# Kernel tuning notes

Measured on AMD Instinct MI355X. Metric: run time of the kernel, lower is better.

Reference implementation:

```python
import jax, jax.numpy as jnp
import numpy as np

NUM_GRAPHS = 1024


def setup_inputs() -> dict:
    key = jax.random.key(0)
    k1, k2, k3, k4 = jax.random.split(key, 4)
    N, D, H = 500000, 256, 128
    x = jax.random.normal(k1, (N, D), dtype=jnp.float32)
    # attention MLP params (Linear(D,H) -> ReLU -> Linear(H,1))
    W1 = jax.random.normal(k2, (D, H), dtype=jnp.float32) * (1.0 / np.sqrt(D))
    b1 = jnp.zeros((H,), dtype=jnp.float32)
    W2 = jax.random.normal(k3, (H, 1), dtype=jnp.float32) * (1.0 / np.sqrt(H))
    b2 = jnp.zeros((1,), dtype=jnp.float32)
    batch = jnp.sort(jax.random.randint(k4, (N,), 0, NUM_GRAPHS)).astype(jnp.int64)
    return {"x": x, "W1": W1, "b1": b1, "W2": W2, "b2": b2, "batch": batch}


def reference(x, W1, b1, W2, b2, batch):
    # attention MLP -> scalar score per node, softmax over ALL nodes (global, as in source)
    h = jax.nn.relu(x @ W1 + b1)            # [N, H]
    scores = h @ W2 + b2                    # [N, 1]
    attn = jax.nn.softmax(scores.ravel())[:, None]  # [N, 1], global softmax

    # attention-weighted sum per graph
    attn_pooled = jax.ops.segment_sum(x * attn, batch, num_segments=NUM_GRAPHS,
                                      indices_are_sorted=True)  # [G, D]
    # max pool per graph (all segments occupied given N >> G)
    max_pooled = jax.ops.segment_max(x, batch, num_segments=NUM_GRAPHS,
                                     indices_are_sorted=True)   # [G, D]
    # mean pool per graph: scatter-add + clamped counts
    sum_pooled = jax.ops.segment_sum(x, batch, num_segments=NUM_GRAPHS,
                                     indices_are_sorted=True)   # [G, D]
    counts = jnp.bincount(batch, length=NUM_GRAPHS).astype(x.dtype)
    counts = jnp.clip(counts, 1.0, None)[:, None]                # [G, 1]
    mean_pooled = sum_pooled / counts

    return jnp.concatenate([attn_pooled, max_pooled, mean_pooled], axis=-1)  # [G, 3D]
```

## Files before the change

kernel.cpp:

```cpp
#include <hip/hip_runtime.h>
#include <cmath>

#define D_IN 256
#define H_DIM 128
#define NUM_GRAPHS 1024
#define CHUNK 32
#define MAXSEG 2
#define REC_F 768

typedef __attribute__((ext_vector_type(8))) __bf16 bf16x8;
typedef __attribute__((ext_vector_type(4))) float f32x4;

__device__ inline void load_lds_16(const void* g, void* l) {
    __builtin_amdgcn_global_load_lds(
        (const __attribute__((address_space(1))) void*)g,
        (__attribute__((address_space(3))) void*)l, 16, 0, 0);
}

__device__ inline int lower_bound_i(const int* __restrict__ arr, int n, int val) {
    int lo = 0, hi = n;
    while (lo < hi) {
        int mid = (lo + hi) >> 1;
        if (arr[mid] < val) lo = mid + 1; else hi = mid;
    }
    return lo;
}

__global__ __launch_bounds__(256) void prep_kernel(
    const float* __restrict__ W1, const int* __restrict__ batch, int N,
    ushort* __restrict__ packed, int* __restrict__ bounds) {
    int b = blockIdx.x;
    if (b < 16) {
        int tid = b * 256 + threadIdx.x;
        int nt = tid >> 9;
        int ks = (tid >> 6) & 7;
        int l = tid & 63;
        int col = nt * 16 + (l & 15);
        int kbase = ks * 32 + ((l >> 4) & 3) * 8;
#pragma unroll
        for (int i = 0; i < 8; ++i) {
            float v = W1[(size_t)(kbase + i) * H_DIM + col];
            __bf16 h = (__bf16)v;
            packed[(size_t)tid * 8 + i] = __builtin_bit_cast(unsigned short, h);
        }
    } else {
        int i = (b - 16) * 256 + threadIdx.x;
        if (i <= NUM_GRAPHS) bounds[i] = lower_bound_i(batch, N, i);
    }
}

__global__ __launch_bounds__(256, 4) void fused_kernel(
    const float* __restrict__ x, const ushort* __restrict__ w1p,
    const float* __restrict__ b1, const float* __restrict__ W2,
    const float* __restrict__ b2, const int* __restrict__ batch,
    float* __restrict__ recs, float* __restrict__ zpart, int N) {
    int tid = threadIdx.x;
    int l = tid & 63;
    int w = tid >> 6;
    int r16 = l & 15;
    int kg = l >> 4;
    int blk = blockIdx.x;
    long long base = (long long)blk * CHUNK;
    int chunkN = (int)min((long long)CHUNK, (long long)N - base);

    __shared__ float sxf[CHUNK * D_IN];
    __shared__ float pscore[4][CHUNK];
    __shared__ int seglist[MAXSEG + 1];
    __shared__ int snseg;

#pragma unroll
    for (int k = 0; k < 8; ++k) {
        int row = k * 4 + w;
        long long grow = base + row;
        if (grow >= N) grow = N - 1;
        unsigned srcb = ((unsigned)(l * 16)) ^ ((unsigned)(row & 7) << 4);
        const float* src = x + grow * D_IN + (srcb >> 2);
        char* dst = (char*)sxf + (unsigned)(row * 1024 + l * 16);
        load_lds_16(src, dst);
    }

    bf16x8 breg0[8], breg1[8];
#pragma unroll
    for (int ks = 0; ks < 8; ++ks) {
        breg0[ks] = *(const bf16x8*)(w1p + ((size_t)((w * 2) * 8 + ks) * 64 + l) * 8);
        breg1[ks] = *(const bf16x8*)(w1p + ((size_t)((w * 2 + 1) * 8 + ks) * 64 + l) * 8);
    }

    if (w == 0) {
        int bval = -1;
        if (l < chunkN) bval = batch[base + l];
        int prev = __shfl_up(bval, 1, 64);
        bool flag = (l < chunkN) && (l == 0 || bval != prev);
        unsigned long long m = __ballot(flag);
        if (l == 0) {
            int ns = 0;
            while (m && ns < MAXSEG) {
                seglist[ns] = __ffsll(m) - 1;
                ns++;
                m &= m - 1;
            }
            snseg = ns;
            seglist[ns] = chunkN;
        }
    }

    float w2v[2], b1v[2];
#pragma unroll
    for (int q = 0; q < 2; ++q) {
        int c = (w * 2 + q) * 16 + r16;
        w2v[q] = W2[c];
        b1v[q] = b1[c];
    }
    float bb = b2[0];

    __syncthreads();

    f32x4 acc[2][2] = {};
#pragma unroll
    for (int ks = 0; ks < 8; ++ks) {
#pragma unroll
        for (int mt = 0; mt < 2; ++mt) {
            int row = mt * 16 + r16;
            unsigned swz = (unsigned)(row & 7) << 4;
            unsigned cb = (unsigned)(ks * 128 + kg * 32);
            f32x4 u0 = *(const f32x4*)((const char*)sxf + row * 1024 + (cb ^ swz));
            f32x4 u1 = *(const f32x4*)((const char*)sxf + row * 1024 + ((cb + 16) ^ swz));
            bf16x8 af;
#pragma unroll
            for (int i = 0; i < 4; ++i) {
                af[i] = (__bf16)u0[i];
                af[i + 4] = (__bf16)u1[i];
            }
            acc[mt][0] = __builtin_amdgcn_mfma_f32_16x16x32_bf16(af, breg0[ks], acc[mt][0], 0, 0, 0);
            acc[mt][1] = __builtin_amdgcn_mfma_f32_16x16x32_bf16(af, breg1[ks], acc[mt][1], 0, 0, 0);
        }
    }
#pragma unroll
    for (int mt = 0; mt < 2; ++mt) {
#pragma unroll
        for (int reg = 0; reg < 4; ++reg) {
            float p = fmaxf(acc[mt][0][reg] + b1v[0], 0.f) * w2v[0] +
                      fmaxf(acc[mt][1][reg] + b1v[1], 0.f) * w2v[1];
            p += __shfl_xor(p, 1, 64);
            p += __shfl_xor(p, 2, 64);
            p += __shfl_xor(p, 4, 64);
            p += __shfl_xor(p, 8, 64);
            if (r16 == 0) pscore[w][mt * 16 + kg * 4 + reg] = p;
        }
    }
    __syncthreads();

    float e_l = 0.f;
    if (l < CHUNK) {
        float s = pscore[0][l] + pscore[1][l] + pscore[2][l] + pscore[3][l] + bb;
        e_l = (l < chunkN) ? __expf(s) : 0.f;
    }
    if (w == 0) {
        float z = e_l;
        z += __shfl_xor(z, 1, 64);
        z += __shfl_xor(z, 2, 64);
        z += __shfl_xor(z, 4, 64);
        z += __shfl_xor(z, 8, 64);
        z += __shfl_xor(z, 16, 64);
        z += __shfl_xor(z, 32, 64);
        if (l == 0) zpart[blk] = z;
    }

    int nseg = snseg;

    int cg = l & 15;
    int rg = l >> 4;
    unsigned cbyte = (unsigned)(w * 256 + cg * 16);

    for (int sg = 0; sg < nseg; ++sg) {
        int sStart = seglist[sg];
        int sEnd = seglist[sg + 1];
        f32x4 asum = {0.f, 0.f, 0.f, 0.f};
        f32x4 ssum = {0.f, 0.f, 0.f, 0.f};
        f32x4 mx = {-INFINITY, -INFINITY, -INFINITY, -INFINITY};
#pragma unroll
        for (int j = 0; j < 8; ++j) {
            int row = rg + 4 * j;
            float wj = __shfl(e_l, row, 64);
            bool in = (row >= sStart) && (row < sEnd);
            unsigned addr = (unsigned)(row * 1024) +
                            (cbyte ^ ((unsigned)(row & 7) << 4));
            f32x4 v = *(const f32x4*)((const char*)sxf + addr);
            float wje = in ? wj : 0.f;
#pragma unroll
            for (int c = 0; c < 4; ++c) {
                asum[c] += v[c] * wje;
                ssum[c] += in ? v[c] : 0.f;
                mx[c] = fmaxf(mx[c], in ? v[c] : -INFINITY);
            }
        }
#pragma unroll
        for (int c = 0; c < 4; ++c) {
            asum[c] += __shfl_xor(asum[c], 16, 64);
            asum[c] += __shfl_xor(asum[c], 32, 64);
            ssum[c] += __shfl_xor(ssum[c], 16, 64);
            ssum[c] += __shfl_xor(ssum[c], 32, 64);
            mx[c] = fmaxf(mx[c], __shfl_xor(mx[c], 16, 64));
            mx[c] = fmaxf(mx[c], __shfl_xor(mx[c], 32, 64));
        }
        if (rg == 0) {
            float* rb = recs + (size_t)(blk * MAXSEG + sg) * REC_F;
            int co = w * 64 + cg * 4;
            *(f32x4*)(rb + co) = asum;
            *(f32x4*)(rb + 256 + co) = ssum;
            *(f32x4*)(rb + 512 + co) = mx;
        }
    }
}

__global__ __launch_bounds__(256) void combine_kernel(
    const float* __restrict__ recs, const int* __restrict__ bounds,
    const int* __restrict__ batch, const float* __restrict__ zpart, int nzp,
    float* __restrict__ out) {
    int g = blockIdx.x;
    int tid = threadIdx.x;

    __shared__ float szr[256];
    float z = 0.f;
    for (int i = tid; i < nzp; i += 256) z += zpart[i];
    szr[tid] = z;
    __syncthreads();
    for (int off = 128; off > 0; off >>= 1) {
        if (tid < off) szr[tid] += szr[tid + off];
        __syncthreads();
    }
    float invZ = 1.f / szr[0];

    int start = bounds[g];
    int end = bounds[g + 1];
    int cnt = end - start;

    float ew = 0.f, ss = 0.f, mxv = -INFINITY;
    if (cnt > 0) {
        int b0 = start / CHUNK, b1 = (end - 1) / CHUNK;
        int sg0 = (batch[(long long)b0 * CHUNK] == g) ? 0 : 1;
        for (int b = b0; b <= b1; ++b) {
            int sg = (b == b0) ? sg0 : 0;
            const float* rb = recs + (size_t)(b * MAXSEG + sg) * REC_F;
            ew += rb[tid];
            ss += rb[256 + tid];
            mxv = fmaxf(mxv, rb[512 + tid]);
        }
    }
    size_t ob = (size_t)g * (3 * D_IN);
    out[ob + tid] = ew * invZ;
    out[ob + D_IN + tid] = (cnt > 0) ? mxv : 0.f;
    out[ob + 2 * D_IN + tid] = ss / (float)max(cnt, 1);
}

extern "C" void kernel_launch(void* const* d_in, const int* in_sizes, int n_in,
                              void* d_out, int out_size, void* d_ws, size_t ws_size,
                              hipStream_t stream) {
    const float* x = (const float*)d_in[0];
    const float* W1 = (const float*)d_in[1];
    const float* b1 = (const float*)d_in[2];
    const float* W2 = (const float*)d_in[3];
    const float* b2 = (const float*)d_in[4];
    const int* batch = (const int*)d_in[5];
    int N = in_sizes[0] / D_IN;
    float* out = (float*)d_out;
    int NB = (N + CHUNK - 1) / CHUNK;

    char* ws = (char*)d_ws;
    size_t off = 0;
    ushort* w1p = (ushort*)(ws + off);
    off += 8 * 8 * 64 * 8 * sizeof(ushort);
    off = (off + 255) & ~(size_t)255;
    int* bounds = (int*)(ws + off);
    off += (NUM_GRAPHS + 1) * sizeof(int);
    off = (off + 255) & ~(size_t)255;
    float* recs = (float*)(ws + off);
    off += (size_t)NB * MAXSEG * REC_F * sizeof(float);
    off = (off + 255) & ~(size_t)255;
    float* zpart = (float*)(ws + off);
    off += (size_t)NB * sizeof(float);

    prep_kernel<<<21, 256, 0, stream>>>(W1, batch, N, w1p, bounds);
    fused_kernel<<<NB, 256, 0, stream>>>(x, w1p, b1, W2, b2, batch,
                                         recs, zpart, N);
    combine_kernel<<<NUM_GRAPHS, 256, 0, stream>>>(recs, bounds, batch,
                                                   zpart, NB, out);
}
```

Before: 174.8 us.

## Make fused kernel persistent with double-buffered LDS prefetch of chunks

Replaces the one-block-per-32-row-chunk launch with 512 persistent blocks of 512 threads, each looping over a contiguous range of chunks. While the current chunk is being scored and pooled, the next chunk's rows and batch ids are loaded into a second LDS buffer. W1 fragments are loaded into registers once per block instead of once per chunk, and each wave now handles one 16-column N-tile. Softmax partial sums are accumulated per block, which shrinks the zpart reduction in the combine kernel. The cost is 64KB of LDS per block and fewer resident blocks per CU, so fewer loads may be in flight at once.

```diff
diff --git a/kernel.cpp b/kernel.cpp
--- a/kernel.cpp
+++ b/kernel.cpp
@@ -6,6 +6,7 @@
 #define NUM_GRAPHS 1024
 #define CHUNK 32
 #define MAXSEG 2
+#define NPERS 512
 #define REC_F 768
 
 typedef __attribute__((ext_vector_type(8))) __bf16 bf16x8;
@@ -15,6 +16,12 @@
     __builtin_amdgcn_global_load_lds(
         (const __attribute__((address_space(1))) void*)g,
         (__attribute__((address_space(3))) void*)l, 16, 0, 0);
+}
+
+__device__ inline void bar_lds() {
+    asm volatile("s_waitcnt lgkmcnt(0)" ::: "memory");
+    __builtin_amdgcn_s_barrier();
+    asm volatile("" ::: "memory");
 }
 
 __device__ inline int lower_bound_i(const int* __restrict__ arr, int n, int val) {
@@ -49,168 +56,201 @@
     }
 }
 
-__global__ __launch_bounds__(256, 4) void fused_kernel(
+__global__ __launch_bounds__(512) void fused_kernel(
     const float* __restrict__ x, const ushort* __restrict__ w1p,
     const float* __restrict__ b1, const float* __restrict__ W2,
     const float* __restrict__ b2, const int* __restrict__ batch,
-    float* __restrict__ recs, float* __restrict__ zpart, int N) {
+    float* __restrict__ recs, float* __restrict__ zpart, int N, int NB, int K) {
     int tid = threadIdx.x;
     int l = tid & 63;
     int w = tid >> 6;
     int r16 = l & 15;
     int kg = l >> 4;
-    int blk = blockIdx.x;
-    long long base = (long long)blk * CHUNK;
-    int chunkN = (int)min((long long)CHUNK, (long long)N - base);
-
-    __shared__ float sxf[CHUNK * D_IN];
-    __shared__ float pscore[4][CHUNK];
-    __shared__ int seglist[MAXSEG + 1];
-    __shared__ int snseg;
-
-#pragma unroll
-    for (int k = 0; k < 8; ++k) {
-        int row = k * 4 + w;
-        long long grow = base + row;
-        if (grow >= N) grow = N - 1;
-        unsigned srcb = ((unsigned)(l * 16)) ^ ((unsigned)(row & 7) << 4);
-        const float* src = x + grow * D_IN + (srcb >> 2);
-        char* dst = (char*)sxf + (unsigned)(row * 1024 + l * 16);
-        load_lds_16(src, dst);
-    }
-
-    bf16x8 breg0[8], breg1[8];
-#pragma unroll
-    for (int ks = 0; ks < 8; ++ks) {
-        breg0[ks] = *(const bf16x8*)(w1p + ((size_t)((w * 2) * 8 + ks) * 64 + l) * 8);
-        breg1[ks] = *(const bf16x8*)(w1p + ((size_t)((w * 2 + 1) * 8 + ks) * 64 + l) * 8);
-    }
-
+    int c0 = blockIdx.x * K;
+    if (c0 >= NB) {
+        if (tid == 0) zpart[blockIdx.x] = 0.f;
+        return;
+    }
+    int cEnd = min(c0 + K, NB);
+
+    __shared__ float sxf[2][CHUNK * D_IN];
+    __shared__ float pscore[8][CHUNK];
+    __shared__ int seglist[2][MAXSEG + 1];
+    __shared__ int snseg[2];
+
+    bf16x8 breg[8];
+#pragma unroll
+    for (int ks = 0; ks < 8; ++ks)
+        breg[ks] = *(const bf16x8*)(w1p + ((size_t)(w * 8 + ks) * 64 + l) * 8);
+    float w2v = W2[w * 16 + r16];
+    float b1v = b1[w * 16 + r16];
+    float bb = b2[0];
+
+    int cg = l & 7;
+    int rg = l >> 3;
+    unsigned cbyte = (unsigned)(w * 128 + cg * 16);
+
+    float zacc = 0.f;
+
+    {
+        long long base = (long long)c0 * CHUNK;
+#pragma unroll
+        for (int k = 0; k < 4; ++k) {
+            int row = k * 8 + w;
+            long long grow = base + row;
+            if (grow >= N) grow = N - 1;
+            unsigned srcb = ((unsigned)(l * 16)) ^ ((unsigned)(row & 7) << 4);
+            load_lds_16(x + grow * D_IN + (srcb >> 2),
+                        (char*)sxf[0] + (unsigned)(row * 1024 + l * 16));
+        }
+    }
+    int bvalCur = -1;
     if (w == 0) {
-        int bval = -1;
-        if (l < chunkN) bval = batch[base + l];
-        int prev = __shfl_up(bval, 1, 64);
-        bool flag = (l < chunkN) && (l == 0 || bval != prev);
-        unsigned long long m = __ballot(flag);
-        if (l == 0) {
-            int ns = 0;
-            while (m && ns < MAXSEG) {
-                seglist[ns] = __ffsll(m) - 1;
-                ns++;
-                m &= m - 1;
-            }
-            snseg = ns;
-            seglist[ns] = chunkN;
-        }
-    }
-
-    float w2v[2], b1v[2];
-#pragma unroll
-    for (int q = 0; q < 2; ++q) {
-        int c = (w * 2 + q) * 16 + r16;
-        w2v[q] = W2[c];
-        b1v[q] = b1[c];
-    }
-    float bb = b2[0];
-
-    __syncthreads();
-
-    f32x4 acc[2][2] = {};
-#pragma unroll
-    for (int ks = 0; ks < 8; ++ks) {
+        long long bi = (long long)c0 * CHUNK + l;
+        if (l < CHUNK && bi < N) bvalCur = batch[bi];
+    }
+
+    int par = 0;
+    for (int t = c0; t < cEnd; ++t) {
+        long long base = (long long)t * CHUNK;
+        int chunkN = (int)min((long long)CHUNK, (long long)N - base);
+        const float* P = sxf[par];
+
+        __syncthreads();
+
+        int bvalNext = -1;
+        if (t + 1 < cEnd) {
+            long long nbase = base + CHUNK;
+#pragma unroll
+            for (int k = 0; k < 4; ++k) {
+                int row = k * 8 + w;
+                long long grow = nbase + row;
+                if (grow >= N) grow = N - 1;
+                unsigned srcb = ((unsigned)(l * 16)) ^ ((unsigned)(row & 7) << 4);
+                load_lds_16(x + grow * D_IN + (srcb >> 2),
+                            (char*)sxf[par ^ 1] + (unsigned)(row * 1024 + l * 16));
+            }
+            if (w == 0) {
+                long long bi = nbase + l;
+                if (l < CHUNK && bi < N) bvalNext = batch[bi];
+            }
+        }
+
+        if (w == 0) {
+            int prev = __shfl_up(bvalCur, 1, 64);
+            bool flag = (l < chunkN) && (l == 0 || bvalCur != prev);
+            unsigned long long m = __ballot(flag);
+            if (l == 0) {
+                int ns = 0;
+                while (m && ns < MAXSEG) {
+                    seglist[par][ns] = __ffsll(m) - 1;
+                    ns++;
+                    m &= m - 1;
+                }
+                snseg[par] = ns;
+                seglist[par][ns] = chunkN;
+            }
+        }
+
+        f32x4 acc[2] = {};
+#pragma unroll
+        for (int ks = 0; ks < 8; ++ks) {
+#pragma unroll
+            for (int mt = 0; mt < 2; ++mt) {
+                int row = mt * 16 + r16;
+                unsigned swz = (unsigned)(row & 7) << 4;
+                unsigned cb = (unsigned)(ks * 128 + kg * 32);
+                f32x4 u0 = *(const f32x4*)((const char*)P + row * 1024 + (cb ^ swz));
+                f32x4 u1 = *(const f32x4*)((const char*)P + row * 1024 + ((cb + 16) ^ swz));
+                bf16x8 af;
+#pragma unroll
+                for (int i = 0; i < 4; ++i) {
+                    af[i] = (__bf16)u0[i];
+                    af[i + 4] = (__bf16)u1[i];
+                }
+                acc[mt] = __builtin_amdgcn_mfma_f32_16x16x32_bf16(af, breg[ks], acc[mt], 0, 0, 0);
+            }
+        }
 #pragma unroll
         for (int mt = 0; mt < 2; ++mt) {
-            int row = mt * 16 + r16;
-            unsigned swz = (unsigned)(row & 7) << 4;
-            unsigned cb = (unsigned)(ks * 128 + kg * 32);
-            f32x4 u0 = *(const f32x4*)((const char*)sxf + row * 1024 + (cb ^ swz));
-            f32x4 u1 = *(const f32x4*)((const char*)sxf + row * 1024 + ((cb + 16) ^ swz));
-            bf16x8 af;
-#pragma unroll
-            for (int i = 0; i < 4; ++i) {
-                af[i] = (__bf16)u0[i];
-                af[i + 4] = (__bf16)u1[i];
-            }
-            acc[mt][0] = __builtin_amdgcn_mfma_f32_16x16x32_bf16(af, breg0[ks], acc[mt][0], 0, 0, 0);
-            acc[mt][1] = __builtin_amdgcn_mfma_f32_16x16x32_bf16(af, breg1[ks], acc[mt][1], 0, 0, 0);
-        }
-    }
-#pragma unroll
-    for (int mt = 0; mt < 2; ++mt) {
-#pragma unroll
-        for (int reg = 0; reg < 4; ++reg) {
-            float p = fmaxf(acc[mt][0][reg] + b1v[0], 0.f) * w2v[0] +
-                      fmaxf(acc[mt][1][reg] + b1v[1], 0.f) * w2v[1];
-            p += __shfl_xor(p, 1, 64);
-            p += __shfl_xor(p, 2, 64);
-            p += __shfl_xor(p, 4, 64);
-            p += __shfl_xor(p, 8, 64);
-            if (r16 == 0) pscore[w][mt * 16 + kg * 4 + reg] = p;
-        }
-    }
-    __syncthreads();
-
-    float e_l = 0.f;
-    if (l < CHUNK) {
-        float s = pscore[0][l] + pscore[1][l] + pscore[2][l] + pscore[3][l] + bb;
-        e_l = (l < chunkN) ? __expf(s) : 0.f;
-    }
-    if (w == 0) {
-        float z = e_l;
-        z += __shfl_xor(z, 1, 64);
-        z += __shfl_xor(z, 2, 64);
-        z += __shfl_xor(z, 4, 64);
-        z += __shfl_xor(z, 8, 64);
-        z += __shfl_xor(z, 16, 64);
-        z += __shfl_xor(z, 32, 64);
-        if (l == 0) zpart[blk] = z;
-    }
-
-    int nseg = snseg;
-
-    int cg = l & 15;
-    int rg = l >> 4;
-    unsigned cbyte = (unsigned)(w * 256 + cg * 16);
-
-    for (int sg = 0; sg < nseg; ++sg) {
-        int sStart = seglist[sg];
-        int sEnd = seglist[sg + 1];
-        f32x4 asum = {0.f, 0.f, 0.f, 0.f};
-        f32x4 ssum = {0.f, 0.f, 0.f, 0.f};
-        f32x4 mx = {-INFINITY, -INFINITY, -INFINITY, -INFINITY};
-#pragma unroll
-        for (int j = 0; j < 8; ++j) {
-            int row = rg + 4 * j;
-            float wj = __shfl(e_l, row, 64);
-            bool in = (row >= sStart) && (row < sEnd);
-            unsigned addr = (unsigned)(row * 1024) +
-                            (cbyte ^ ((unsigned)(row & 7) << 4));
-            f32x4 v = *(const f32x4*)((const char*)sxf + addr);
-            float wje = in ? wj : 0.f;
+#pragma unroll
+            for (int reg = 0; reg < 4; ++reg) {
+                float p = fmaxf(acc[mt][reg] + b1v, 0.f) * w2v;
+                p += __shfl_xor(p, 1, 64);
+                p += __shfl_xor(p, 2, 64);
+                p += __shfl_xor(p, 4, 64);
+                p += __shfl_xor(p, 8, 64);
+                if (r16 == 0) pscore[w][mt * 16 + kg * 4 + reg] = p;
+            }
+        }
+
+        bar_lds();
+
+        int lr = l & 31;
+        float s = bb;
+#pragma unroll
+        for (int wv = 0; wv < 8; ++wv) s += pscore[wv][lr];
+        float e_l = (l < chunkN) ? __expf(s) : 0.f;
+        if (w == 0) {
+            float z = e_l;
+            z += __shfl_xor(z, 1, 64);
+            z += __shfl_xor(z, 2, 64);
+            z += __shfl_xor(z, 4, 64);
+            z += __shfl_xor(z, 8, 64);
+            z += __shfl_xor(z, 16, 64);
+            z += __shfl_xor(z, 32, 64);
+            if (l == 0) zacc += z;
+        }
+
+        int nseg = snseg[par];
+        for (int sg = 0; sg < nseg; ++sg) {
+            int sStart = seglist[par][sg];
+            int sEnd = seglist[par][sg + 1];
+            f32x4 asum = {0.f, 0.f, 0.f, 0.f};
+            f32x4 ssum = {0.f, 0.f, 0.f, 0.f};
+            f32x4 mx = {-INFINITY, -INFINITY, -INFINITY, -INFINITY};
+#pragma unroll
+            for (int j = 0; j < 4; ++j) {
+                int row = rg + 8 * j;
+                float wj = __shfl(e_l, row, 64);
+                bool in = (row >= sStart) && (row < sEnd);
+                unsigned addr = (unsigned)(row * 1024) +
+                                (cbyte ^ ((unsigned)(row & 7) << 4));
+                f32x4 v = *(const f32x4*)((const char*)P + addr);
+                float wje = in ? wj : 0.f;
+#pragma unroll
+                for (int c = 0; c < 4; ++c) {
+                    asum[c] += v[c] * wje;
+                    ssum[c] += in ? v[c] : 0.f;
+                    mx[c] = fmaxf(mx[c], in ? v[c] : -INFINITY);
+                }
+            }
 #pragma unroll
             for (int c = 0; c < 4; ++c) {
-                asum[c] += v[c] * wje;
-                ssum[c] += in ? v[c] : 0.f;
-                mx[c] = fmaxf(mx[c], in ? v[c] : -INFINITY);
-            }
-        }
-#pragma unroll
-        for (int c = 0; c < 4; ++c) {
-            asum[c] += __shfl_xor(asum[c], 16, 64);
-            asum[c] += __shfl_xor(asum[c], 32, 64);
-            ssum[c] += __shfl_xor(ssum[c], 16, 64);
-            ssum[c] += __shfl_xor(ssum[c], 32, 64);
-            mx[c] = fmaxf(mx[c], __shfl_xor(mx[c], 16, 64));
-            mx[c] = fmaxf(mx[c], __shfl_xor(mx[c], 32, 64));
-        }
-        if (rg == 0) {
-            float* rb = recs + (size_t)(blk * MAXSEG + sg) * REC_F;
-            int co = w * 64 + cg * 4;
-            *(f32x4*)(rb + co) = asum;
-            *(f32x4*)(rb + 256 + co) = ssum;
-            *(f32x4*)(rb + 512 + co) = mx;
-        }
-    }
+                asum[c] += __shfl_xor(asum[c], 8, 64);
+                asum[c] += __shfl_xor(asum[c], 16, 64);
+                asum[c] += __shfl_xor(asum[c], 32, 64);
+                ssum[c] += __shfl_xor(ssum[c], 8, 64);
+                ssum[c] += __shfl_xor(ssum[c], 16, 64);
+                ssum[c] += __shfl_xor(ssum[c], 32, 64);
+                mx[c] = fmaxf(mx[c], __shfl_xor(mx[c], 8, 64));
+                mx[c] = fmaxf(mx[c], __shfl_xor(mx[c], 16, 64));
+                mx[c] = fmaxf(mx[c], __shfl_xor(mx[c], 32, 64));
+            }
+            if (rg == 0) {
+                float* rb = recs + (size_t)(t * MAXSEG + sg) * REC_F;
+                int co = w * 32 + cg * 4;
+                *(f32x4*)(rb + co) = asum;
+                *(f32x4*)(rb + 256 + co) = ssum;
+                *(f32x4*)(rb + 512 + co) = mx;
+            }
+        }
+
+        bvalCur = bvalNext;
+        par ^= 1;
+    }
+
+    if (w == 0 && l == 0) zpart[blockIdx.x] = zacc;
 }
 
 __global__ __launch_bounds__(256) void combine_kernel(
@@ -265,6 +305,7 @@
     int N = in_sizes[0] / D_IN;
     float* out = (float*)d_out;
     int NB = (N + CHUNK - 1) / CHUNK;
+    int K = (NB + NPERS - 1) / NPERS;
 
     char* ws = (char*)d_ws;
     size_t off = 0;
@@ -278,11 +319,11 @@
     off += (size_t)NB * MAXSEG * REC_F * sizeof(float);
     off = (off + 255) & ~(size_t)255;
     float* zpart = (float*)(ws + off);
-    off += (size_t)NB * sizeof(float);
+    off += (size_t)NPERS * sizeof(float);
 
     prep_kernel<<<21, 256, 0, stream>>>(W1, batch, N, w1p, bounds);
-    fused_kernel<<<NB, 256, 0, stream>>>(x, w1p, b1, W2, b2, batch,
-                                         recs, zpart, N);
+    fused_kernel<<<NPERS, 512, 0, stream>>>(x, w1p, b1, W2, b2, batch,
+                                            recs, zpart, N, NB, K);
     combine_kernel<<<NUM_GRAPHS, 256, 0, stream>>>(recs, bounds, batch,
-                                                   zpart, NB, out);
-}
+                                                   zpart, NPERS, out);
+}
```

New measurement: 325.7 us. +86.3%, slower.
